# Optimization experiments

Hardware: AMD Instinct MI355X
Metric: run time of the kernel (lower is better)

Reference implementation:

```python
import jax, jax.numpy as jnp
import numpy as np

N_SPECIES = 8
MAX_RADIAL = 16
D_IN = MAX_RADIAL * N_SPECIES        # 128: max_radial * n_species (property axis)
N_COMBINED = 256                     # n_combined_basis
M = 131072                           # total stacked (samples x components) rows across all blocks


def setup_inputs() -> dict:
    key = jax.random.key(0)
    k1, k2, k3 = jax.random.split(key, 3)
    values = jax.random.normal(k1, (M, D_IN), dtype=jnp.float32)
    species_idx = jax.random.randint(k2, (M,), 0, N_SPECIES, dtype=jnp.int32)
    # torch.rand -> uniform [0, 1)
    combining_matrix = jax.random.uniform(k3, (N_SPECIES, D_IN, N_COMBINED), dtype=jnp.float32)
    return {"values": values, "species_idx": species_idx, "combining_matrix": combining_matrix}


def reference(values, species_idx, combining_matrix):
    # Grouped GEMM: each row uses the weight slice of its central species.
    # Loop over the small fixed species set (not a data dim); mask + accumulate
    # avoids materializing a per-row [M, D_IN, N_COMBINED] weight gather.
    out = jnp.zeros((values.shape[0], combining_matrix.shape[2]), dtype=values.dtype)
    for s in range(combining_matrix.shape[0]):
        mask = (species_idx == s)[:, None]                  # [M, 1]
        out = out + jnp.where(mask, values @ combining_matrix[s], 0.0)
    return out
```

## Files before the change

kernel.cpp:

```cpp
#include <hip/hip_runtime.h>
#include <stdint.h>

#define MROWS 131072
#define NSPEC 8
#define DIN   128
#define NOUT  256
#define BM    256

typedef __attribute__((ext_vector_type(8))) short s16x8;
typedef __attribute__((ext_vector_type(4))) float f32x4;

#define OFF_BF    ((size_t)0)
#define WS_NEEDED ((size_t)524288)

__device__ __forceinline__ uint32_t bf16_1(float f) {
  union { float f; uint32_t u; } v; v.f = f;
  return (v.u + 0x7FFFu + ((v.u >> 16) & 1u)) >> 16;
}

__global__ void k_convert(const float* __restrict__ B, char* __restrict__ ws) {
  int gid = blockIdx.x * 256 + threadIdx.x;
  int l  = gid & 63;
  int c  = gid >> 6;
  int kt = c & 3;
  int f  = (c >> 2) & 15;
  int s  = c >> 6;
  int n  = (f >> 2) * 64 + (l & 15) * 4 + (f & 3);
  int k0 = kt * 32 + (l >> 4) * 8;
  const float* src = B + (size_t)s * DIN * NOUT + n;
  uint32_t w0 = bf16_1(src[(size_t)(k0 + 0) * NOUT]) | (bf16_1(src[(size_t)(k0 + 1) * NOUT]) << 16);
  uint32_t w1 = bf16_1(src[(size_t)(k0 + 2) * NOUT]) | (bf16_1(src[(size_t)(k0 + 3) * NOUT]) << 16);
  uint32_t w2 = bf16_1(src[(size_t)(k0 + 4) * NOUT]) | (bf16_1(src[(size_t)(k0 + 5) * NOUT]) << 16);
  uint32_t w3 = bf16_1(src[(size_t)(k0 + 6) * NOUT]) | (bf16_1(src[(size_t)(k0 + 7) * NOUT]) << 16);
  *(uint4*)(ws + OFF_BF + (size_t)c * 1024 + (size_t)l * 16) = make_uint4(w0, w1, w2, w3);
}

__global__ __launch_bounds__(256, 2) void k_gemm_ns(const float* __restrict__ A,
                                                    const int* __restrict__ sp,
                                                    const char* __restrict__ ws,
                                                    float* __restrict__ out) {
  const char* Bf = ws + OFF_BF;
  __shared__ char As[BM * 256];
  __shared__ int slotOf[BM];
  __shared__ int invOf[BM];
  __shared__ int cnt[NSPEC];
  __shared__ int gstart[NSPEC + 1];

  int t = threadIdx.x;
  int base = blockIdx.x * BM;

  if (t < NSPEC) cnt[t] = 0;
  __syncthreads();
  int s_r = sp[base + t] & 7;
  int rank = atomicAdd(&cnt[s_r], 1);
  __syncthreads();
  if (t == 0) {
    int a = 0;
    #pragma unroll
    for (int j = 0; j < NSPEC; ++j) { gstart[j] = a; a += cnt[j]; }
    gstart[NSPEC] = a;
  }
  __syncthreads();
  int myslot = gstart[s_r] + rank;
  slotOf[t] = myslot;
  invOf[myslot] = t;
  __syncthreads();

  int f4 = t & 31, r0 = t >> 5;
  #pragma unroll
  for (int it = 0; it < 32; ++it) {
    int r = r0 + it * 8;
    float4 v = *(const float4*)(A + (size_t)(base + r) * DIN + f4 * 4);
    int sl = slotOf[r];
    uint32_t lo = bf16_1(v.x) | (bf16_1(v.y) << 16);
    uint32_t hi = bf16_1(v.z) | (bf16_1(v.w) << 16);
    int off = (sl * 256 + f4 * 8) ^ ((sl & 7) << 4);
    *(uint2*)(As + off) = make_uint2(lo, hi);
  }
  __syncthreads();

  int w = t >> 6, l = t & 63;
  int colBase = w * 64 + (l & 15) * 4;
  for (int s = 0; s < NSPEC; ++s) {
    int gs = gstart[s], ge = gstart[s + 1];
    if (gs == ge) continue;
    s16x8 bfr[4][4];
    #pragma unroll
    for (int ni = 0; ni < 4; ++ni)
      #pragma unroll
      for (int kt = 0; kt < 4; ++kt) {
        int c = (s * 16 + (w * 4 + ni)) * 4 + kt;
        bfr[ni][kt] = *(const s16x8*)(Bf + (size_t)c * 1024 + (size_t)l * 16);
      }
    int st0 = gs >> 4, st1 = (ge - 1) >> 4;
    for (int st = st0; st <= st1; ++st) {
      f32x4 acc[4];
      #pragma unroll
      for (int ni = 0; ni < 4; ++ni) acc[ni] = (f32x4){0.f, 0.f, 0.f, 0.f};
      #pragma unroll
      for (int kt = 0; kt < 4; ++kt) {
        int r = st * 16 + (l & 15);
        int off = (r * 256 + kt * 64 + (l >> 4) * 16) ^ ((r & 7) << 4);
        s16x8 afr = *(const s16x8*)(As + off);
        #pragma unroll
        for (int ni = 0; ni < 4; ++ni)
          acc[ni] = __builtin_amdgcn_mfma_f32_16x16x32_bf16(afr, bfr[ni][kt], acc[ni], 0, 0, 0);
      }
      #pragma unroll
      for (int q = 0; q < 4; ++q) {
        int slotrow = st * 16 + ((l >> 4) << 2) + q;
        if (slotrow >= gs && slotrow < ge) {
          int rid = base + invOf[slotrow];
          float4 v4 = make_float4(acc[0][q], acc[1][q], acc[2][q], acc[3][q]);
          *(float4*)(out + (size_t)rid * NOUT + colBase) = v4;
        }
      }
    }
  }
}

__global__ void k_naive(const float* __restrict__ A, const int* __restrict__ sp,
                        const float* __restrict__ B, float* __restrict__ out) {
  __shared__ float av[DIN];
  int m = blockIdx.x;
  int n = threadIdx.x;
  if (n < DIN) av[n] = A[(size_t)m * DIN + n];
  __syncthreads();
  int s = sp[m] & 7;
  const float* b = B + (size_t)s * DIN * NOUT + n;
  float acc = 0.f;
  #pragma unroll 8
  for (int k = 0; k < DIN; ++k) acc = fmaf(av[k], b[(size_t)k * NOUT], acc);
  out[(size_t)m * NOUT + n] = acc;
}

extern "C" void kernel_launch(void* const* d_in, const int* in_sizes, int n_in,
                              void* d_out, int out_size, void* d_ws, size_t ws_size,
                              hipStream_t stream) {
  const float* values = (const float*)d_in[0];
  const int*   sp     = (const int*)d_in[1];
  const float* B      = (const float*)d_in[2];
  float*       out    = (float*)d_out;

  if (d_ws == nullptr || ws_size < WS_NEEDED) {
    k_naive<<<MROWS, NOUT, 0, stream>>>(values, sp, B, out);
    return;
  }
  char* ws = (char*)d_ws;
  k_convert<<<128, 256, 0, stream>>>(B, ws);
  k_gemm_ns<<<MROWS / BM, 256, 0, stream>>>(values, sp, ws, out);
}
```

Measured before the change: 42.59 us.

## Pipeline A-tile loads in 64-slot chunks overlapping compute via register double buffering

The A tile is now gathered in sorted slot order through invOf and loaded in four 64-row chunks into two register buffers. Each chunk's conversion and LDS write is followed by a custom barrier that waits only on LDS counters, so the next chunk's global loads stay in flight while the MFMA compute for the current chunk runs. Compute walks 16-row subtiles, finds which species fall in each, and reloads B fragments only when the species changes. The cost is more registers (16 float4 buffers) and the risk of lower occupancy, plus extra species-range logic per subtile.

```diff
diff --git a/kernel.cpp b/kernel.cpp
--- a/kernel.cpp
+++ b/kernel.cpp
@@ -35,13 +35,18 @@
   *(uint4*)(ws + OFF_BF + (size_t)c * 1024 + (size_t)l * 16) = make_uint4(w0, w1, w2, w3);
 }
 
+__device__ __forceinline__ void bar_keep_vmem() {
+  asm volatile("s_waitcnt lgkmcnt(0)" ::: "memory");
+  __builtin_amdgcn_s_barrier();
+  __builtin_amdgcn_sched_barrier(0);
+}
+
 __global__ __launch_bounds__(256, 2) void k_gemm_ns(const float* __restrict__ A,
                                                     const int* __restrict__ sp,
                                                     const char* __restrict__ ws,
                                                     float* __restrict__ out) {
   const char* Bf = ws + OFF_BF;
   __shared__ char As[BM * 256];
-  __shared__ int slotOf[BM];
   __shared__ int invOf[BM];
   __shared__ int cnt[NSPEC];
   __shared__ int gstart[NSPEC + 1];
@@ -61,62 +66,94 @@
     gstart[NSPEC] = a;
   }
   __syncthreads();
-  int myslot = gstart[s_r] + rank;
-  slotOf[t] = myslot;
-  invOf[myslot] = t;
+  invOf[gstart[s_r] + rank] = t;
   __syncthreads();
 
-  int f4 = t & 31, r0 = t >> 5;
-  #pragma unroll
-  for (int it = 0; it < 32; ++it) {
-    int r = r0 + it * 8;
-    float4 v = *(const float4*)(A + (size_t)(base + r) * DIN + f4 * 4);
-    int sl = slotOf[r];
-    uint32_t lo = bf16_1(v.x) | (bf16_1(v.y) << 16);
-    uint32_t hi = bf16_1(v.z) | (bf16_1(v.w) << 16);
-    int off = (sl * 256 + f4 * 8) ^ ((sl & 7) << 4);
-    *(uint2*)(As + off) = make_uint2(lo, hi);
-  }
-  __syncthreads();
-
+  int f4 = t & 31;
+  int r8 = t >> 5;
   int w = t >> 6, l = t & 63;
   int colBase = w * 64 + (l & 15) * 4;
-  for (int s = 0; s < NSPEC; ++s) {
-    int gs = gstart[s], ge = gstart[s + 1];
-    if (gs == ge) continue;
-    s16x8 bfr[4][4];
+
+  float4 ra[8], rb[8];
+  s16x8 bfr[4][4];
+  int cur = -1;
+
+  auto LD = [&](float4 (&reg)[8], int c) {
     #pragma unroll
-    for (int ni = 0; ni < 4; ++ni)
+    for (int j = 0; j < 8; ++j) {
+      int slot = c * 64 + r8 + j * 8;
+      int row = invOf[slot];
+      reg[j] = *(const float4*)(A + (size_t)(base + row) * DIN + f4 * 4);
+    }
+  };
+  auto WR = [&](float4 (&reg)[8], int c) {
+    #pragma unroll
+    for (int j = 0; j < 8; ++j) {
+      int slot = c * 64 + r8 + j * 8;
+      uint32_t lo = bf16_1(reg[j].x) | (bf16_1(reg[j].y) << 16);
+      uint32_t hi = bf16_1(reg[j].z) | (bf16_1(reg[j].w) << 16);
+      int off = (slot * 256 + f4 * 8) ^ ((slot & 7) << 4);
+      *(uint2*)(As + off) = make_uint2(lo, hi);
+    }
+  };
+  auto CMP = [&](int c) {
+    for (int st = c * 4; st < c * 4 + 4; ++st) {
+      int r16 = st * 16;
+      int slo = 0, shi = 0;
       #pragma unroll
-      for (int kt = 0; kt < 4; ++kt) {
-        int c = (s * 16 + (w * 4 + ni)) * 4 + kt;
-        bfr[ni][kt] = *(const s16x8*)(Bf + (size_t)c * 1024 + (size_t)l * 16);
+      for (int j = 1; j < NSPEC; ++j) {
+        if (r16 >= gstart[j]) slo = j;
+        if (r16 + 15 >= gstart[j]) shi = j;
       }
-    int st0 = gs >> 4, st1 = (ge - 1) >> 4;
-    for (int st = st0; st <= st1; ++st) {
-      f32x4 acc[4];
-      #pragma unroll
-      for (int ni = 0; ni < 4; ++ni) acc[ni] = (f32x4){0.f, 0.f, 0.f, 0.f};
-      #pragma unroll
-      for (int kt = 0; kt < 4; ++kt) {
-        int r = st * 16 + (l & 15);
-        int off = (r * 256 + kt * 64 + (l >> 4) * 16) ^ ((r & 7) << 4);
-        s16x8 afr = *(const s16x8*)(As + off);
+      for (int s = slo; s <= shi; ++s) {
+        int gs = gstart[s], ge = gstart[s + 1];
+        if (ge <= gs) continue;
+        if (s != cur) {
+          cur = s;
+          #pragma unroll
+          for (int ni = 0; ni < 4; ++ni)
+            #pragma unroll
+            for (int kt = 0; kt < 4; ++kt)
+              bfr[ni][kt] = *(const s16x8*)(Bf +
+                  (size_t)((s * 16 + (w * 4 + ni)) * 4 + kt) * 1024 + (size_t)l * 16);
+        }
+        f32x4 acc[4];
         #pragma unroll
-        for (int ni = 0; ni < 4; ++ni)
-          acc[ni] = __builtin_amdgcn_mfma_f32_16x16x32_bf16(afr, bfr[ni][kt], acc[ni], 0, 0, 0);
-      }
-      #pragma unroll
-      for (int q = 0; q < 4; ++q) {
-        int slotrow = st * 16 + ((l >> 4) << 2) + q;
-        if (slotrow >= gs && slotrow < ge) {
-          int rid = base + invOf[slotrow];
-          float4 v4 = make_float4(acc[0][q], acc[1][q], acc[2][q], acc[3][q]);
-          *(float4*)(out + (size_t)rid * NOUT + colBase) = v4;
+        for (int ni = 0; ni < 4; ++ni) acc[ni] = (f32x4){0.f, 0.f, 0.f, 0.f};
+        #pragma unroll
+        for (int kt = 0; kt < 4; ++kt) {
+          int rr = r16 + (l & 15);
+          int off = (rr * 256 + kt * 64 + (l >> 4) * 16) ^ ((rr & 7) << 4);
+          s16x8 afr = *(const s16x8*)(As + off);
+          #pragma unroll
+          for (int ni = 0; ni < 4; ++ni)
+            acc[ni] = __builtin_amdgcn_mfma_f32_16x16x32_bf16(afr, bfr[ni][kt], acc[ni], 0, 0, 0);
+        }
+        #pragma unroll
+        for (int q = 0; q < 4; ++q) {
+          int slotrow = r16 + ((l >> 4) << 2) + q;
+          if (slotrow >= gs && slotrow < ge) {
+            int rid = base + invOf[slotrow];
+            float4 v4 = make_float4(acc[0][q], acc[1][q], acc[2][q], acc[3][q]);
+            *(float4*)(out + (size_t)rid * NOUT + colBase) = v4;
+          }
         }
       }
     }
-  }
+  };
+
+  LD(ra, 0);
+  LD(rb, 1);
+  WR(ra, 0); bar_keep_vmem();
+  LD(ra, 2);
+  CMP(0);
+  WR(rb, 1); bar_keep_vmem();
+  LD(rb, 3);
+  CMP(1);
+  WR(ra, 2); bar_keep_vmem();
+  CMP(2);
+  WR(rb, 3); bar_keep_vmem();
+  CMP(3);
 }
 
 __global__ void k_naive(const float* __restrict__ A, const int* __restrict__ sp,
```

Result: slower. 44.92 us (+5.5%).
